# Kernel tuning notes

Hardware: AMD Instinct MI355X
Metric: run time of the kernel (lower is better)

## Reference

```python
import jax, jax.numpy as jnp
import numpy as np

N_MET = 250_000
N_RXN = 500_000
E_SUB = 2_000_000
E_ALL = 4_000_000
HIDDEN = 64
MSG_DIM = 32
DT = 0.01  # flux-limiting step size (forward called with dt > 0)


def setup_inputs() -> dict:
    key = jax.random.key(0)
    ks = jax.random.split(key, 12)
    inp = {}
    inp["x"] = jax.random.uniform(ks[0], (N_MET, 8), dtype=jnp.float32)
    inp["met_sub"] = jax.random.randint(ks[1], (E_SUB,), 0, N_MET, dtype=jnp.int32)
    inp["rxn_sub"] = jax.random.randint(ks[2], (E_SUB,), 0, N_RXN, dtype=jnp.int32)
    inp["sto_sub"] = jax.random.uniform(ks[3], (E_SUB,), dtype=jnp.float32) + 0.5  # |s_ij| > 0
    inp["met_all"] = jax.random.randint(ks[4], (E_ALL,), 0, N_MET, dtype=jnp.int32)
    inp["rxn_all"] = jax.random.randint(ks[5], (E_ALL,), 0, N_RXN, dtype=jnp.int32)
    inp["sto_all"] = jax.random.normal(ks[6], (E_ALL,), dtype=jnp.float32)
    sc = lambda fan_in: 1.0 / np.sqrt(fan_in)
    inp["W1"] = jax.random.normal(ks[7], (2, HIDDEN), dtype=jnp.float32) * sc(2)
    inp["b1"] = jnp.zeros((HIDDEN,), jnp.float32)
    inp["W2"] = jax.random.normal(ks[8], (HIDDEN, MSG_DIM), dtype=jnp.float32) * sc(HIDDEN)
    inp["b2"] = jnp.zeros((MSG_DIM,), jnp.float32)
    inp["W3"] = jax.random.normal(ks[9], (MSG_DIM, HIDDEN), dtype=jnp.float32) * sc(MSG_DIM)
    inp["b3"] = jnp.zeros((HIDDEN,), jnp.float32)
    inp["W4"] = jax.random.normal(ks[10], (HIDDEN, 1), dtype=jnp.float32) * sc(HIDDEN)
    inp["b4"] = jnp.zeros((1,), jnp.float32)
    inp["log_k"] = jax.random.uniform(ks[11], (N_RXN,), dtype=jnp.float32, minval=-3.0, maxval=-1.0)
    return inp


def reference(x, met_sub, rxn_sub, sto_sub, met_all, rxn_all, sto_all,
              W1, b1, W2, b2, W3, b3, W4, b4, log_k):
    conc = x[:, 3]                                            # [n_met]
    # per-substrate-edge message: MLP([conc_src, |s|]) -> msg_dim
    msg_in = jnp.stack([conc[met_sub], sto_sub], axis=-1)     # [E_sub, 2]
    msg = jnp.tanh(msg_in @ W1 + b1) @ W2 + b2                # [E_sub, msg_dim]
    # aggregate messages per reaction (index_add)
    h_rxn = jax.ops.segment_sum(msg, rxn_sub, num_segments=N_RXN)  # [n_rxn, msg_dim]
    # non-negative rates
    k = jnp.power(10.0, log_k)
    r = (jnp.tanh(h_rxn @ W3 + b3) @ W4 + b4)[:, 0]           # [n_rxn]
    v = k * jax.nn.softplus(r)
    # flux limiting: scale rates so no substrate is over-consumed in one dt step
    consumption = sto_sub * v[rxn_sub] * DT                   # [E_sub]
    total = jax.ops.segment_sum(consumption, met_sub, num_segments=N_MET)
    active = total > 1e-12
    met_scale = jnp.where(active,
                          jnp.minimum(conc / jnp.where(active, total, 1.0), 1.0),
                          1.0)                                # [n_met]
    edge_scale = met_scale[met_sub]
    rxn_scale = jnp.ones((N_RXN,), v.dtype).at[rxn_sub].min(edge_scale)  # amin, include_self
    v = v * rxn_scale
    # dx/dt = scatter-add of signed stoich * rate over all edges
    contrib = sto_all * v[rxn_all]                            # [E_all]
    dxdt = jax.ops.segment_sum(contrib, met_all, num_segments=N_MET)
    return dxdt[:, None]                                      # [n_met, 1]
```

## Files before the change

### kernel.cpp

```cpp
#include <hip/hip_runtime.h>

#define N_MET 250000
#define N_RXN 500000
#define N_RXN_PAD 500032
#define E_SUB 2000000
#define E_ALL 4000000
#define DT 0.01f

#define RXN_PER_BLK 256
#define THREADS 256
#define EDGE_CAP 1536

#define MV_RPB 64

#define BINSZ 1024
#define NBINS ((N_MET + BINSZ - 1) / BINSZ)
#define PART_EPB 4096
#define PTHREADS 512
#define KPB (PART_EPB / PTHREADS)
#define PART_NBLK ((E_ALL + PART_EPB - 1) / PART_EPB)
#define SPART_NBLK ((E_SUB + PART_EPB - 1) / PART_EPB)
#define RBINSZ 1024
#define RNBINS ((N_RXN + RBINSZ - 1) / RBINSZ)
#define RPART_NBLK ((E_SUB + PART_EPB - 1) / PART_EPB)
#define RBIN_CAP 6144

typedef int v4i __attribute__((ext_vector_type(4)));
typedef float v4f __attribute__((ext_vector_type(4)));
typedef short bf16x8 __attribute__((ext_vector_type(8)));
typedef float f32x4 __attribute__((ext_vector_type(4)));

#if __has_builtin(__builtin_amdgcn_exp2f)
#define EXP2F(x) __builtin_amdgcn_exp2f(x)
#else
#define EXP2F(x) exp2f(x)
#endif
#if __has_builtin(__builtin_amdgcn_rcpf)
#define RCPF(x) __builtin_amdgcn_rcpf(x)
#else
#define RCPF(x) __fdividef(1.0f, (x))
#endif

static __device__ __forceinline__ float fast_tanh(float x) {
  float e = __expf(x + x);
  return 1.0f - __fdividef(2.0f, e + 1.0f);
}

static __device__ __forceinline__ int bcast_i(int v, int lane) {
  return __builtin_amdgcn_readlane(v, lane);
}

static __device__ __forceinline__ unsigned short bf16_rn(float f) {
  unsigned u = __float_as_uint(f);
  unsigned r = u + 0x7FFFu + ((u >> 16) & 1u);
  return (unsigned short)(r >> 16);
}

__global__ __launch_bounds__(256) void k_bc3(
    const int* __restrict__ rxn_sub, const int* __restrict__ met_sub,
    const int* __restrict__ met_all,
    const float* __restrict__ x, float* __restrict__ conc,
    const float* __restrict__ W2, const float* __restrict__ W3,
    const float* __restrict__ b2,
    uint4* __restrict__ wfh, uint4* __restrict__ wfl, float* __restrict__ b2w3,
    int* __restrict__ rblk_cnt, int* __restrict__ sblk_cnt, int* __restrict__ blk_cnt) {
  __shared__ int cnt[RNBINS];
  int b = blockIdx.x, t = threadIdx.x;
  const int* keys; int nkeys, nblk, nb, bl; int* out;
  if (b < RPART_NBLK) {
    keys = rxn_sub; nkeys = E_SUB; nblk = RPART_NBLK; nb = RNBINS; out = rblk_cnt; bl = b;
    if (b < 2) {
      int tid = b * 256 + t;
      if (tid < 512) {
        int lane = tid & 63, jt = (tid >> 6) & 3, ks = tid >> 8;
        int jj = jt * 16 + (lane & 15);
        unsigned short h[8], l[8];
        #pragma unroll
        for (int q = 0; q < 8; ++q) {
          int kk = ks * 32 + (lane >> 4) * 8 + q;
          float w = 0.f;
          #pragma unroll
          for (int m = 0; m < 32; ++m) w = fmaf(W2[kk * 32 + m], W3[m * 64 + jj], w);
          h[q] = bf16_rn(w);
          float hf = __uint_as_float(((unsigned)h[q]) << 16);
          l[q] = bf16_rn(w - hf);
        }
        uint4 H, L;
        H.x = (unsigned)h[0] | ((unsigned)h[1] << 16);
        H.y = (unsigned)h[2] | ((unsigned)h[3] << 16);
        H.z = (unsigned)h[4] | ((unsigned)h[5] << 16);
        H.w = (unsigned)h[6] | ((unsigned)h[7] << 16);
        L.x = (unsigned)l[0] | ((unsigned)l[1] << 16);
        L.y = (unsigned)l[2] | ((unsigned)l[3] << 16);
        L.z = (unsigned)l[4] | ((unsigned)l[5] << 16);
        L.w = (unsigned)l[6] | ((unsigned)l[7] << 16);
        int idx = (ks * 4 + jt) * 64 + lane;
        wfh[idx] = H; wfl[idx] = L;
      }
      if (tid < 64) {
        float s = 0.f;
        #pragma unroll
        for (int m = 0; m < 32; ++m) s = fmaf(b2[m], W3[m * 64 + tid], s);
        b2w3[tid] = s;
      }
    }
  } else if (b < RPART_NBLK + SPART_NBLK) {
    keys = met_sub; nkeys = E_SUB; nblk = SPART_NBLK; nb = NBINS; out = sblk_cnt;
    bl = b - RPART_NBLK;
  } else {
    keys = met_all; nkeys = E_ALL; nblk = PART_NBLK; nb = NBINS; out = blk_cnt;
    bl = b - RPART_NBLK - SPART_NBLK;
    int m = bl * 256 + t;
    if (m < N_MET) conc[m] = __builtin_nontemporal_load(x + m * 8 + 3);
  }
  for (int i = t; i < nb; i += 256) cnt[i] = 0;
  __syncthreads();
  int base = bl * PART_EPB;
  #pragma unroll
  for (int i = 0; i < PART_EPB / 256; ++i) {
    int e = base + i * 256 + t;
    if (e < nkeys) atomicAdd(&cnt[__builtin_nontemporal_load(keys + e) >> 10], 1);
  }
  __syncthreads();
  for (int i = t; i < nb; i += 256) out[i * nblk + bl] = cnt[i];
}

static __device__ __forceinline__ void scan1_body(int* ss,
    const int* __restrict__ blk_cnt, int* __restrict__ blk_pref,
    int* __restrict__ bin_tot, int nblk, int j) {
  int t = threadIdx.x;
  int carry = 0;
  for (int c = 0; c < nblk; c += 256) {
    int idx = c + t;
    int v = (idx < nblk) ? blk_cnt[j * nblk + idx] : 0;
    ss[t] = v; __syncthreads();
    for (int d = 1; d < 256; d <<= 1) {
      int a = (t >= d) ? ss[t - d] : 0;
      __syncthreads();
      ss[t] += a;
      __syncthreads();
    }
    if (idx < nblk) blk_pref[j * nblk + idx] = carry + ss[t] - v;
    carry += ss[255];
    __syncthreads();
  }
  if (t == 0) bin_tot[j] = carry;
}

__global__ __launch_bounds__(256) void k_scan1all(
    const int* __restrict__ rblk_cnt, int* __restrict__ rblk_pref, int* __restrict__ rbin_tot,
    const int* __restrict__ sblk_cnt, int* __restrict__ sblk_pref, int* __restrict__ sbin_tot,
    const int* __restrict__ blk_cnt, int* __restrict__ blk_pref, int* __restrict__ bin_tot) {
  __shared__ int ss[256];
  int b = blockIdx.x;
  if (b < RNBINS)
    scan1_body(ss, rblk_cnt, rblk_pref, rbin_tot, RPART_NBLK, b);
  else if (b < RNBINS + NBINS)
    scan1_body(ss, sblk_cnt, sblk_pref, sbin_tot, SPART_NBLK, b - RNBINS);
  else
    scan1_body(ss, blk_cnt, blk_pref, bin_tot, PART_NBLK, b - RNBINS - NBINS);
}

__global__ __launch_bounds__(512) void k_scan2all(
    const int* __restrict__ rbin_tot, int* __restrict__ rbin_start,
    const int* __restrict__ sbin_tot, int* __restrict__ sbin_start,
    const int* __restrict__ bin_tot, int* __restrict__ bin_start) {
  __shared__ int ss[512];
  const int* tot; int* st; int n;
  if (blockIdx.x == 0)      { tot = rbin_tot; st = rbin_start; n = RNBINS; }
  else if (blockIdx.x == 1) { tot = sbin_tot; st = sbin_start; n = NBINS; }
  else                      { tot = bin_tot;  st = bin_start;  n = NBINS; }
  int t = threadIdx.x;
  int v = (t < n) ? tot[t] : 0;
  ss[t] = v; __syncthreads();
  for (int d = 1; d < 512; d <<= 1) {
    int a = (t >= d) ? ss[t - d] : 0;
    __syncthreads();
    ss[t] += a;
    __syncthreads();
  }
  if (t < n) st[t] = ss[t] - v;
}

template <int NB, bool PACK, typename MakeRec>
static __device__ __forceinline__ void part_sorted(
    const int* __restrict__ keys, int nkeys, int nblk,
    const int* __restrict__ blk_pref, const int* __restrict__ bin_start,
    int2* __restrict__ out, MakeRec make) {
  __shared__ int2 ordered[PART_EPB];
  __shared__ unsigned short binb[PACK ? 1 : PART_EPB];
  __shared__ int cnt[NB];
  __shared__ int gofs[NB];
  __shared__ int ss[PTHREADS];
  int b = blockIdx.x, t = threadIdx.x;
  for (int i = t; i < NB; i += PTHREADS) cnt[i] = 0;
  __syncthreads();
  int base = b * PART_EPB;
  int kbuf[KPB];
  #pragma unroll
  for (int i = 0; i < KPB; ++i) {
    int e = base + i * PTHREADS + t;
    kbuf[i] = (e < nkeys) ? __builtin_nontemporal_load(keys + e) : -1;
    if (kbuf[i] >= 0) atomicAdd(&cnt[kbuf[i] >> 10], 1);
  }
  __syncthreads();
  int v = (t < NB) ? cnt[t] : 0;
  ss[t] = v; __syncthreads();
  for (int d = 1; d < PTHREADS; d <<= 1) {
    int a = (t >= d) ? ss[t - d] : 0;
    __syncthreads();
    ss[t] += a;
    __syncthreads();
  }
  int nloc = ss[PTHREADS - 1];
  if (t < NB) {
    int ls = ss[t] - v;
    cnt[t] = ls;
    gofs[t] = bin_start[t] + blk_pref[t * nblk + b] - ls;
  }
  __syncthreads();
  #pragma unroll
  for (int i = 0; i < KPB; ++i) {
    int k = kbuf[i];
    if (k >= 0) {
      int e = base + i * PTHREADS + t;
      int bin = k >> 10;
      int2 rec = make(e, k);
      int pos = atomicAdd(&cnt[bin], 1);
      ordered[pos] = rec;
      if (!PACK) binb[pos] = (unsigned short)bin;
    }
  }
  __syncthreads();
  for (int i = t; i < nloc; i += PTHREADS) {
    int2 rec = ordered[i];
    int bin = PACK ? (int)(((unsigned)rec.x) >> 10) : (int)binb[i];
    out[gofs[bin] + i] = rec;
  }
}

__global__ __launch_bounds__(PTHREADS) void k_rpart(
    const int* __restrict__ rxn_sub, const int* __restrict__ met_sub,
    const float* __restrict__ sto_sub,
    const int* __restrict__ blk_pref, const int* __restrict__ bin_start,
    int2* __restrict__ bins_rxn) {
  part_sorted<RNBINS, false>(rxn_sub, E_SUB, RPART_NBLK, blk_pref, bin_start, bins_rxn,
    [=] __device__ (int e, int k) {
      int m = __builtin_nontemporal_load(met_sub + e);
      float st = __builtin_nontemporal_load(sto_sub + e);
      int2 rec; rec.x = ((k & (RBINSZ - 1)) << 18) | m; rec.y = __float_as_int(st);
      return rec;
    });
}

__global__ __launch_bounds__(PTHREADS) void k_part_sub(
    const int* __restrict__ met_sub, const int* __restrict__ rxn_sub,
    const float* __restrict__ sto_sub, const float* __restrict__ v_pre,
    const int* __restrict__ blk_pref, const int* __restrict__ bin_start,
    int2* __restrict__ bins_sub) {
  part_sorted<NBINS, true>(met_sub, E_SUB, SPART_NBLK, blk_pref, bin_start, bins_sub,
    [=] __device__ (int e, int k) {
      int r = __builtin_nontemporal_load(rxn_sub + e);
      float st = __builtin_nontemporal_load(sto_sub + e);
      float val = st * v_pre[r] * DT;
      int2 rec; rec.x = k; rec.y = __float_as_int(val);
      return rec;
    });
}

__global__ __launch_bounds__(PTHREADS) void k_part(
    const int* __restrict__ met_all, const int* __restrict__ rxn_all,
    const float* __restrict__ sto_all, const float* __restrict__ vfin,
    const int* __restrict__ blk_pref, const int* __restrict__ bin_start,
    int2* __restrict__ bins) {
  part_sorted<NBINS, true>(met_all, E_ALL, PART_NBLK, blk_pref, bin_start, bins,
    [=] __device__ (int e, int k) {
      int r = __builtin_nontemporal_load(rxn_all + e);
      float st = __builtin_nontemporal_load(sto_all + e);
      float val = st * vfin[r];
      int2 rec; rec.x = k; rec.y = __float_as_int(val);
      return rec;
    });
}

__global__ __launch_bounds__(256) void k_rbin(
    const int2* __restrict__ bins_rxn, const int* __restrict__ rbin_start,
    const int* __restrict__ rbin_tot, int2* __restrict__ edges8, int* __restrict__ off) {
  __shared__ int2 stage[RBIN_CAP];
  __shared__ int lcnt[RBINSZ];
  __shared__ int lcur[RBINSZ];
  __shared__ int ss[256];
  int j = blockIdx.x, t = threadIdx.x;
  int base = rbin_start[j], n = rbin_tot[j];
  for (int i = t; i < RBINSZ; i += 256) lcnt[i] = 0;
  __syncthreads();
  bool fits = (n <= RBIN_CAP);
  if (fits) {
    for (int i = t; i < n; i += 256) {
      int2 rec = bins_rxn[base + i];
      stage[i] = rec;
      atomicAdd(&lcnt[((unsigned)rec.x) >> 18], 1);
    }
  } else {
    for (int i = t; i < n; i += 256) {
      int2 rec = bins_rxn[base + i];
      atomicAdd(&lcnt[((unsigned)rec.x) >> 18], 1);
    }
  }
  __syncthreads();
  int s0 = lcnt[4 * t], s1 = lcnt[4 * t + 1], s2 = lcnt[4 * t + 2], s3 = lcnt[4 * t + 3];
  int tsum = s0 + s1 + s2 + s3;
  ss[t] = tsum; __syncthreads();
  for (int d = 1; d < 256; d <<= 1) {
    int a = (t >= d) ? ss[t - d] : 0;
    __syncthreads();
    ss[t] += a;
    __syncthreads();
  }
  int run = ss[t] - tsum;
  lcur[4 * t] = run;
  lcur[4 * t + 1] = run + s0;
  lcur[4 * t + 2] = run + s0 + s1;
  lcur[4 * t + 3] = run + s0 + s1 + s2;
  __syncthreads();
  int R0 = j * RBINSZ;
  for (int rl = t; rl < RBINSZ; rl += 256) {
    int r = R0 + rl;
    if (r < N_RXN) off[r] = base + lcur[rl];
  }
  if (j == 0 && t == 0) off[N_RXN] = E_SUB;
  __syncthreads();
  if (fits) {
    for (int i = t; i < n; i += 256) {
      int2 rec = stage[i];
      int pos = atomicAdd(&lcur[((unsigned)rec.x) >> 18], 1);
      int2 out; out.x = rec.x & 0x3FFFF; out.y = rec.y;
      edges8[base + pos] = out;
    }
  } else {
    for (int i = t; i < n; i += 256) {
      int2 rec = bins_rxn[base + i];
      int pos = atomicAdd(&lcur[((unsigned)rec.x) >> 18], 1);
      int2 out; out.x = rec.x & 0x3FFFF; out.y = rec.y;
      edges8[base + pos] = out;
    }
  }
}

static __device__ __forceinline__ float edge_rsum_lds(int o0, int o1, int estart,
                                                      const float2* ep,
                                                      float w1x, float w1y, float b1j) {
  float S0 = 0.f, S1 = 0.f;
  int c = o0;
  for (; c + 1 < o1; c += 2) {
    float2 e0 = ep[c - estart];
    float2 e1 = ep[c + 1 - estart];
    float t0 = fmaf(e0.x, w1x, fmaf(e0.y, w1y, b1j));
    float t1 = fmaf(e1.x, w1x, fmaf(e1.y, w1y, b1j));
    S0 += RCPF(EXP2F(t0) + 1.0f);
    S1 += RCPF(EXP2F(t1) + 1.0f);
  }
  if (c < o1) {
    float2 e0 = ep[c - estart];
    float t0 = fmaf(e0.x, w1x, fmaf(e0.y, w1y, b1j));
    S0 += RCPF(EXP2F(t0) + 1.0f);
  }
  return S0 + S1;
}

static __device__ __forceinline__ float edge_rsum_glob(int o0, int o1,
                                                       const int2* edges8,
                                                       const float* conc,
                                                       float w1x, float w1y, float b1j) {
  float S = 0.f;
  for (int c = o0; c < o1; ++c) {
    int2 rec = edges8[c];
    float cc = conc[rec.x];
    float t0 = fmaf(cc, w1x, fmaf(__int_as_float(rec.y), w1y, b1j));
    S += RCPF(EXP2F(t0) + 1.0f);
  }
  return S;
}

__global__ __launch_bounds__(THREADS) void k_edge(
    const int* __restrict__ off, const int2* __restrict__ edges8,
    const float* __restrict__ conc,
    const float* __restrict__ W1, const float* __restrict__ b1,
    unsigned short* __restrict__ Thi, unsigned short* __restrict__ Tlo, int use_lo) {
  __shared__ int off_s[RXN_PER_BLK + 1];
  __shared__ float2 se[EDGE_CAP];

  int tid = threadIdx.x;
  int lane = tid & 63;
  int wv = tid >> 6;
  int R0 = blockIdx.x * RXN_PER_BLK;

  for (int i = tid; i <= RXN_PER_BLK; i += THREADS) {
    int r = R0 + i;
    off_s[i] = off[r > N_RXN ? N_RXN : r];
  }
  __syncthreads();
  int estart = off_s[0];
  int nE = off_s[RXN_PER_BLK] - estart;
  bool fits = (nE <= EDGE_CAP);
  if (fits) {
    for (int i = tid; i < nE; i += THREADS) {
      int2 rec = edges8[estart + i];
      se[i] = make_float2(conc[rec.x], __int_as_float(rec.y));
    }
  }

  const float C2 = 2.8853900817779268f;
  float w1x = W1[lane] * C2, w1y = W1[64 + lane] * C2, b1j = b1[lane] * C2;

  int rbase = R0 + wv * 64;
  int o0l = off_s[wv * 64 + lane];
  int o1l = off_s[wv * 64 + lane + 1];

  __syncthreads();

  int o0 = bcast_i(o0l, 0);
  #pragma clang loop unroll(disable)
  for (int i = 0; i < 64; ++i) {
    int r = rbase + i;
    if (r >= N_RXN) break;
    int o1 = bcast_i(o1l, i);
    float S = fits ? edge_rsum_lds(o0, o1, estart, se, w1x, w1y, b1j)
                   : edge_rsum_glob(o0, o1, edges8, conc, w1x, w1y, b1j);
    float T = (float)(o1 - o0) - 2.0f * S;
    unsigned short hi = bf16_rn(T);
    Thi[r * 64 + lane] = hi;
    if (use_lo) {
      float hf = __uint_as_float(((unsigned)hi) << 16);
      Tlo[r * 64 + lane] = bf16_rn(T - hf);
    }
    o0 = o1;
  }
}

__global__ __launch_bounds__(256) void k_mv(
    const int* __restrict__ off,
    const unsigned short* __restrict__ Thi, const unsigned short* __restrict__ Tlo,
    const uint4* __restrict__ wfh, const uint4* __restrict__ wfl,
    const float* __restrict__ b2w3, const float* __restrict__ b3,
    const float* __restrict__ W4, const float* __restrict__ b4,
    const float* __restrict__ log_k, int use_lo, float* __restrict__ v_pre) {
  __shared__ int soff[MV_RPB + 1];
  int tid = threadIdx.x, lane = tid & 63, w = tid >> 6;
  int B0 = blockIdx.x * MV_RPB;
  for (int i = tid; i <= MV_RPB; i += 256) {
    int r = B0 + i;
    soff[i] = off[r > N_RXN ? N_RXN : r];
  }
  __syncthreads();

  int R0 = B0 + w * 16;
  int col = lane & 15, rowg = lane >> 4;

  bf16x8 ah[2], al[2];
  {
    int rowelem = (R0 + col) * 64 + rowg * 8;
    const uint4* ph = (const uint4*)Thi;
    ah[0] = __builtin_bit_cast(bf16x8, ph[rowelem >> 3]);
    ah[1] = __builtin_bit_cast(bf16x8, ph[(rowelem + 32) >> 3]);
    if (use_lo) {
      const uint4* pl = (const uint4*)Tlo;
      al[0] = __builtin_bit_cast(bf16x8, pl[rowelem >> 3]);
      al[1] = __builtin_bit_cast(bf16x8, pl[(rowelem + 32) >> 3]);
    }
  }

  f32x4 acc[4];
  #pragma unroll
  for (int jt = 0; jt < 4; ++jt) acc[jt] = (f32x4){0.f, 0.f, 0.f, 0.f};

  #pragma unroll
  for (int jt = 0; jt < 4; ++jt) {
    #pragma unroll
    for (int ks = 0; ks < 2; ++ks) {
      int bidx = (ks * 4 + jt) * 64 + lane;
      bf16x8 bh = __builtin_bit_cast(bf16x8, wfh[bidx]);
      acc[jt] = __builtin_amdgcn_mfma_f32_16x16x32_bf16(ah[ks], bh, acc[jt], 0, 0, 0);
      if (use_lo) {
        bf16x8 bl = __builtin_bit_cast(bf16x8, wfl[bidx]);
        acc[jt] = __builtin_amdgcn_mfma_f32_16x16x32_bf16(ah[ks], bl, acc[jt], 0, 0, 0);
        acc[jt] = __builtin_amdgcn_mfma_f32_16x16x32_bf16(al[ks], bh, acc[jt], 0, 0, 0);
      }
    }
  }

  float w4c[4], bwc[4], b3c[4];
  #pragma unroll
  for (int jt = 0; jt < 4; ++jt) {
    int jj = jt * 16 + col;
    w4c[jt] = W4[jj]; bwc[jt] = b2w3[jj]; b3c[jt] = b3[jj];
  }
  float b40 = b4[0];

  float nq[4];
  #pragma unroll
  for (int q = 0; q < 4; ++q) {
    int idx = w * 16 + rowg * 4 + q;
    nq[q] = (float)(soff[idx + 1] - soff[idx]);
  }

  #pragma unroll
  for (int q = 0; q < 4; ++q) {
    float s = 0.f;
    #pragma unroll
    for (int jt = 0; jt < 4; ++jt) {
      float u = acc[jt][q] + nq[q] * bwc[jt] + b3c[jt];
      s += fast_tanh(u) * w4c[jt];
    }
    s += __shfl_xor(s, 1, 64);
    s += __shfl_xor(s, 2, 64);
    s += __shfl_xor(s, 4, 64);
    s += __shfl_xor(s, 8, 64);
    if (col == 0) {
      int r = R0 + rowg * 4 + q;
      float lk = (r < N_RXN) ? log_k[r] : 0.f;
      float racc = s + b40;
      float k10 = __expf(lk * 2.3025850929940457f);
      float sp = (racc > 15.f) ? racc : __logf(1.f + __expf(racc));
      if (r < N_RXN) v_pre[r] = k10 * sp;
    }
  }
}

__global__ __launch_bounds__(512) void k_bins_sub(
    const int2* __restrict__ bins_sub, const int* __restrict__ bin_start,
    const int* __restrict__ bin_tot, const float* __restrict__ conc,
    float* __restrict__ met_scale) {
  __shared__ float acc[BINSZ];
  int j = blockIdx.x, t = threadIdx.x;
  for (int i = t; i < BINSZ; i += 512) acc[i] = 0.f;
  __syncthreads();
  int s0 = bin_start[j], n = bin_tot[j];
  for (int i = t; i < n; i += 512) {
    int2 rec = bins_sub[s0 + i];
    atomicAdd(&acc[rec.x & (BINSZ - 1)], __int_as_float(rec.y));
  }
  __syncthreads();
  int m0 = j * BINSZ;
  for (int i = t; i < BINSZ; i += 512) {
    int m = m0 + i;
    if (m < N_MET) {
      float tot = acc[i];
      met_scale[m] = (tot > 1e-12f) ? fminf(conc[m] / tot, 1.0f) : 1.0f;
    }
  }
}

__global__ __launch_bounds__(256) void k_rscale(
    const int* __restrict__ off, const int2* __restrict__ edges8,
    const float* __restrict__ met_scale, const float* __restrict__ v_pre,
    float* __restrict__ vfin) {
  __shared__ int soff[MV_RPB + 1];
  int tid = threadIdx.x, lane = tid & 63, w = tid >> 6;
  int B0 = blockIdx.x * MV_RPB;
  for (int i = tid; i <= MV_RPB; i += 256) {
    int r = B0 + i;
    soff[i] = off[r > N_RXN ? N_RXN : r];
  }
  __syncthreads();

  int rloc = w * 16 + (lane >> 2);
  int o0 = soff[rloc], o1 = soff[rloc + 1];
  float sc = 1.0f;
  for (int c = o0 + (lane & 3); c < o1; c += 4) {
    sc = fminf(sc, met_scale[edges8[c].x]);
  }
  sc = fminf(sc, __shfl_xor(sc, 1, 64));
  sc = fminf(sc, __shfl_xor(sc, 2, 64));
  if ((lane & 3) == 0) {
    int r = B0 + rloc;
    if (r < N_RXN) vfin[r] = v_pre[r] * sc;
  }
}

__global__ __launch_bounds__(512) void k_bins(const int2* __restrict__ bins,
                                              const int* __restrict__ bin_start,
                                              const int* __restrict__ bin_tot,
                                              float* __restrict__ dxdt) {
  __shared__ float acc[BINSZ];
  int j = blockIdx.x, t = threadIdx.x;
  for (int i = t; i < BINSZ; i += 512) acc[i] = 0.f;
  __syncthreads();
  int s0 = bin_start[j], n = bin_tot[j];
  for (int i = t; i < n; i += 512) {
    int2 rec = bins[s0 + i];
    atomicAdd(&acc[rec.x & (BINSZ - 1)], __int_as_float(rec.y));
  }
  __syncthreads();
  int m0 = j * BINSZ;
  for (int i = t; i < BINSZ; i += 512) {
    int m = m0 + i;
    if (m < N_MET) dxdt[m] = acc[i];
  }
}

extern "C" void kernel_launch(void* const* d_in, const int* in_sizes, int n_in,
                              void* d_out, int out_size, void* d_ws, size_t ws_size,
                              hipStream_t stream) {
  const float* x       = (const float*)d_in[0];
  const int*   met_sub = (const int*)d_in[1];
  const int*   rxn_sub = (const int*)d_in[2];
  const float* sto_sub = (const float*)d_in[3];
  const int*   met_all = (const int*)d_in[4];
  const int*   rxn_all = (const int*)d_in[5];
  const float* sto_all = (const float*)d_in[6];
  const float* W1    = (const float*)d_in[7];
  const float* b1    = (const float*)d_in[8];
  const float* W2    = (const float*)d_in[9];
  const float* b2    = (const float*)d_in[10];
  const float* W3    = (const float*)d_in[11];
  const float* b3    = (const float*)d_in[12];
  const float* W4    = (const float*)d_in[13];
  const float* b4    = (const float*)d_in[14];
  const float* log_k = (const float*)d_in[15];
  float* dxdt = (float*)d_out;

  char* ws = (char*)d_ws;
  size_t p = 0;
  auto alloc = [&](size_t bytes) -> void* {
    void* r = (void*)(ws + p);
    p += (bytes + 255) & ~(size_t)255;
    return r;
  };
  int*    off        = (int*)alloc(sizeof(int) * (N_RXN + 1));
  uint4*  wfh        = (uint4*)alloc(sizeof(uint4) * 512);
  uint4*  wfl        = (uint4*)alloc(sizeof(uint4) * 512);
  float*  b2w3       = (float*)alloc(sizeof(float) * 64);
  float*  v_pre      = (float*)alloc(sizeof(float) * N_RXN);
  float*  vfin       = (float*)alloc(sizeof(float) * N_RXN);
  float*  conc       = (float*)alloc(sizeof(float) * N_MET);
  float*  met_scale  = (float*)alloc(sizeof(float) * N_MET);
  int2*   edges8     = (int2*)alloc(sizeof(int2) * E_SUB);
  int2*   bins_rxn   = (int2*)alloc(sizeof(int2) * E_SUB);
  int2*   bins_sub   = (int2*)alloc(sizeof(int2) * E_SUB);
  int2*   bins       = (int2*)alloc(sizeof(int2) * E_ALL);
  int*    rblk_cnt   = (int*)alloc(sizeof(int) * RNBINS * RPART_NBLK);
  int*    rblk_pref  = (int*)alloc(sizeof(int) * RNBINS * RPART_NBLK);
  int*    sblk_cnt   = (int*)alloc(sizeof(int) * NBINS * SPART_NBLK);
  int*    sblk_pref  = (int*)alloc(sizeof(int) * NBINS * SPART_NBLK);
  int*    blk_cnt    = (int*)alloc(sizeof(int) * NBINS * PART_NBLK);
  int*    blk_pref   = (int*)alloc(sizeof(int) * NBINS * PART_NBLK);
  int*    rbin_tot   = (int*)alloc(sizeof(int) * 512);
  int*    rbin_start = (int*)alloc(sizeof(int) * 512);
  int*    sbin_tot   = (int*)alloc(sizeof(int) * 512);
  int*    sbin_start = (int*)alloc(sizeof(int) * 512);
  int*    bin_tot    = (int*)alloc(sizeof(int) * 512);
  int*    bin_start  = (int*)alloc(sizeof(int) * 512);
  unsigned short* Thi = (unsigned short*)alloc(sizeof(unsigned short) * (size_t)N_RXN_PAD * 64);
  size_t tlo_bytes = sizeof(unsigned short) * (size_t)N_RXN_PAD * 64;
  int use_lo = (p + tlo_bytes <= ws_size) ? 1 : 0;
  unsigned short* Tlo = use_lo ? (unsigned short*)alloc(tlo_bytes) : Thi;
  (void)in_sizes; (void)n_in; (void)out_size;


  k_bc3<<<RPART_NBLK + SPART_NBLK + PART_NBLK, 256, 0, stream>>>(
      rxn_sub, met_sub, met_all, x, conc, W2, W3, b2, wfh, wfl, b2w3,
      rblk_cnt, sblk_cnt, blk_cnt);
  k_scan1all<<<RNBINS + NBINS + NBINS, 256, 0, stream>>>(
      rblk_cnt, rblk_pref, rbin_tot, sblk_cnt, sblk_pref, sbin_tot,
      blk_cnt, blk_pref, bin_tot);
  k_scan2all<<<3, 512, 0, stream>>>(rbin_tot, rbin_start, sbin_tot, sbin_start,
                                    bin_tot, bin_start);

  k_rpart<<<RPART_NBLK, PTHREADS, 0, stream>>>(rxn_sub, met_sub, sto_sub,
                                               rblk_pref, rbin_start, bins_rxn);
  k_rbin<<<RNBINS, 256, 0, stream>>>(bins_rxn, rbin_start, rbin_tot, edges8, off);

  k_edge<<<(N_RXN + RXN_PER_BLK - 1) / RXN_PER_BLK, THREADS, 0, stream>>>(
      off, edges8, conc, W1, b1, Thi, Tlo, use_lo);
  k_mv<<<(N_RXN + MV_RPB - 1) / MV_RPB, 256, 0, stream>>>(
      off, Thi, Tlo, wfh, wfl, b2w3, b3, W4, b4, log_k, use_lo, v_pre);

  k_part_sub<<<SPART_NBLK, PTHREADS, 0, stream>>>(met_sub, rxn_sub, sto_sub, v_pre,
                                                  sblk_pref, sbin_start, bins_sub);
  k_bins_sub<<<NBINS, 512, 0, stream>>>(bins_sub, sbin_start, sbin_tot, conc, met_scale);

  k_rscale<<<(N_RXN + MV_RPB - 1) / MV_RPB, 256, 0, stream>>>(
      off, edges8, met_scale, v_pre, vfin);

  k_part<<<PART_NBLK, PTHREADS, 0, stream>>>(met_all, rxn_all, sto_all, vfin,
                                             blk_pref, bin_start, bins);
  k_bins<<<NBINS, 512, 0, stream>>>(bins, bin_start, bin_tot, dxdt);
}
```

Before: 430.3 us.

## Fuse edge-sum and MFMA rate kernels through per-wave LDS tiles

Merges the per-reaction edge tanh-sum kernel with the MFMA matrix-vector rate kernel. Each wave now writes its 16-reaction T tile (hi and lo bf16 parts) into padded shared memory and runs the MFMAs immediately, so the 500k x 64 bf16 intermediates never go to global memory. This removes a kernel launch and two large global round trips. In exchange the fused kernel uses more LDS and registers, which may lower occupancy, and the lo correction is now always computed.

After: 418.9 us. 1.03x faster.

```diff
diff --git a/kernel.cpp b/kernel.cpp
--- a/kernel.cpp
+++ b/kernel.cpp
@@ -2,7 +2,6 @@
 
 #define N_MET 250000
 #define N_RXN 500000
-#define N_RXN_PAD 500032
 #define E_SUB 2000000
 #define E_ALL 4000000
 #define DT 0.01f
@@ -10,6 +9,7 @@
 #define RXN_PER_BLK 256
 #define THREADS 256
 #define EDGE_CAP 1536
+#define TPAD 72
 
 #define MV_RPB 64
 
@@ -382,13 +382,18 @@
   return S;
 }
 
-__global__ __launch_bounds__(THREADS) void k_edge(
+__global__ __launch_bounds__(THREADS) void k_edge_mv(
     const int* __restrict__ off, const int2* __restrict__ edges8,
     const float* __restrict__ conc,
     const float* __restrict__ W1, const float* __restrict__ b1,
-    unsigned short* __restrict__ Thi, unsigned short* __restrict__ Tlo, int use_lo) {
+    const uint4* __restrict__ wfh, const uint4* __restrict__ wfl,
+    const float* __restrict__ b2w3, const float* __restrict__ b3,
+    const float* __restrict__ W4, const float* __restrict__ b4,
+    const float* __restrict__ log_k, float* __restrict__ v_pre) {
   __shared__ int off_s[RXN_PER_BLK + 1];
   __shared__ float2 se[EDGE_CAP];
+  __shared__ __align__(16) unsigned short thi[4][16][TPAD];
+  __shared__ __align__(16) unsigned short tlo[4][16][TPAD];
 
   int tid = threadIdx.x;
   int lane = tid & 63;
@@ -417,77 +422,7 @@
   int o0l = off_s[wv * 64 + lane];
   int o1l = off_s[wv * 64 + lane + 1];
 
-  __syncthreads();
-
-  int o0 = bcast_i(o0l, 0);
-  #pragma clang loop unroll(disable)
-  for (int i = 0; i < 64; ++i) {
-    int r = rbase + i;
-    if (r >= N_RXN) break;
-    int o1 = bcast_i(o1l, i);
-    float S = fits ? edge_rsum_lds(o0, o1, estart, se, w1x, w1y, b1j)
-                   : edge_rsum_glob(o0, o1, edges8, conc, w1x, w1y, b1j);
-    float T = (float)(o1 - o0) - 2.0f * S;
-    unsigned short hi = bf16_rn(T);
-    Thi[r * 64 + lane] = hi;
-    if (use_lo) {
-      float hf = __uint_as_float(((unsigned)hi) << 16);
-      Tlo[r * 64 + lane] = bf16_rn(T - hf);
-    }
-    o0 = o1;
-  }
-}
-
-__global__ __launch_bounds__(256) void k_mv(
-    const int* __restrict__ off,
-    const unsigned short* __restrict__ Thi, const unsigned short* __restrict__ Tlo,
-    const uint4* __restrict__ wfh, const uint4* __restrict__ wfl,
-    const float* __restrict__ b2w3, const float* __restrict__ b3,
-    const float* __restrict__ W4, const float* __restrict__ b4,
-    const float* __restrict__ log_k, int use_lo, float* __restrict__ v_pre) {
-  __shared__ int soff[MV_RPB + 1];
-  int tid = threadIdx.x, lane = tid & 63, w = tid >> 6;
-  int B0 = blockIdx.x * MV_RPB;
-  for (int i = tid; i <= MV_RPB; i += 256) {
-    int r = B0 + i;
-    soff[i] = off[r > N_RXN ? N_RXN : r];
-  }
-  __syncthreads();
-
-  int R0 = B0 + w * 16;
   int col = lane & 15, rowg = lane >> 4;
-
-  bf16x8 ah[2], al[2];
-  {
-    int rowelem = (R0 + col) * 64 + rowg * 8;
-    const uint4* ph = (const uint4*)Thi;
-    ah[0] = __builtin_bit_cast(bf16x8, ph[rowelem >> 3]);
-    ah[1] = __builtin_bit_cast(bf16x8, ph[(rowelem + 32) >> 3]);
-    if (use_lo) {
-      const uint4* pl = (const uint4*)Tlo;
-      al[0] = __builtin_bit_cast(bf16x8, pl[rowelem >> 3]);
-      al[1] = __builtin_bit_cast(bf16x8, pl[(rowelem + 32) >> 3]);
-    }
-  }
-
-  f32x4 acc[4];
-  #pragma unroll
-  for (int jt = 0; jt < 4; ++jt) acc[jt] = (f32x4){0.f, 0.f, 0.f, 0.f};
-
-  #pragma unroll
-  for (int jt = 0; jt < 4; ++jt) {
-    #pragma unroll
-    for (int ks = 0; ks < 2; ++ks) {
-      int bidx = (ks * 4 + jt) * 64 + lane;
-      bf16x8 bh = __builtin_bit_cast(bf16x8, wfh[bidx]);
-      acc[jt] = __builtin_amdgcn_mfma_f32_16x16x32_bf16(ah[ks], bh, acc[jt], 0, 0, 0);
-      if (use_lo) {
-        bf16x8 bl = __builtin_bit_cast(bf16x8, wfl[bidx]);
-        acc[jt] = __builtin_amdgcn_mfma_f32_16x16x32_bf16(ah[ks], bl, acc[jt], 0, 0, 0);
-        acc[jt] = __builtin_amdgcn_mfma_f32_16x16x32_bf16(al[ks], bh, acc[jt], 0, 0, 0);
-      }
-    }
-  }
 
   float w4c[4], bwc[4], b3c[4];
   #pragma unroll
@@ -497,32 +432,83 @@
   }
   float b40 = b4[0];
 
-  float nq[4];
-  #pragma unroll
-  for (int q = 0; q < 4; ++q) {
-    int idx = w * 16 + rowg * 4 + q;
-    nq[q] = (float)(soff[idx + 1] - soff[idx]);
-  }
-
-  #pragma unroll
-  for (int q = 0; q < 4; ++q) {
-    float s = 0.f;
+  __syncthreads();
+
+  const uint4* wfh_v = wfh;
+  const uint4* wfl_v = wfl;
+
+  unsigned short* thw = &thi[wv][0][0];
+  unsigned short* tlw = &tlo[wv][0][0];
+
+  int o0 = bcast_i(o0l, 0);
+  #pragma clang loop unroll(disable)
+  for (int tt = 0; tt < 4; ++tt) {
+    asm volatile("" : "+v"(wfh_v), "+v"(wfl_v));
+    int rt = rbase + tt * 16;
+    #pragma clang loop unroll(disable)
+    for (int i = 0; i < 16; ++i) {
+      int li = tt * 16 + i;
+      int o1 = bcast_i(o1l, li);
+      float S = fits ? edge_rsum_lds(o0, o1, estart, se, w1x, w1y, b1j)
+                     : edge_rsum_glob(o0, o1, edges8, conc, w1x, w1y, b1j);
+      float T = (float)(o1 - o0) - 2.0f * S;
+      unsigned short hi = bf16_rn(T);
+      float hf = __uint_as_float(((unsigned)hi) << 16);
+      thw[i * TPAD + lane] = hi;
+      tlw[i * TPAD + lane] = bf16_rn(T - hf);
+      o0 = o1;
+    }
+    bf16x8 ah[2], al[2];
+    {
+      int fo = col * TPAD + rowg * 8;
+      const uint4* ph = (const uint4*)thw;
+      const uint4* pl = (const uint4*)tlw;
+      ah[0] = __builtin_bit_cast(bf16x8, ph[fo >> 3]);
+      ah[1] = __builtin_bit_cast(bf16x8, ph[(fo + 32) >> 3]);
+      al[0] = __builtin_bit_cast(bf16x8, pl[fo >> 3]);
+      al[1] = __builtin_bit_cast(bf16x8, pl[(fo + 32) >> 3]);
+    }
+    f32x4 acc[4];
+    #pragma unroll
+    for (int jt = 0; jt < 4; ++jt) acc[jt] = (f32x4){0.f, 0.f, 0.f, 0.f};
     #pragma unroll
     for (int jt = 0; jt < 4; ++jt) {
-      float u = acc[jt][q] + nq[q] * bwc[jt] + b3c[jt];
-      s += fast_tanh(u) * w4c[jt];
-    }
-    s += __shfl_xor(s, 1, 64);
-    s += __shfl_xor(s, 2, 64);
-    s += __shfl_xor(s, 4, 64);
-    s += __shfl_xor(s, 8, 64);
-    if (col == 0) {
-      int r = R0 + rowg * 4 + q;
-      float lk = (r < N_RXN) ? log_k[r] : 0.f;
-      float racc = s + b40;
-      float k10 = __expf(lk * 2.3025850929940457f);
-      float sp = (racc > 15.f) ? racc : __logf(1.f + __expf(racc));
-      if (r < N_RXN) v_pre[r] = k10 * sp;
+      #pragma unroll
+      for (int ks = 0; ks < 2; ++ks) {
+        int bidx = (ks * 4 + jt) * 64 + lane;
+        bf16x8 bh = __builtin_bit_cast(bf16x8, wfh_v[bidx]);
+        bf16x8 bl = __builtin_bit_cast(bf16x8, wfl_v[bidx]);
+        acc[jt] = __builtin_amdgcn_mfma_f32_16x16x32_bf16(ah[ks], bh, acc[jt], 0, 0, 0);
+        acc[jt] = __builtin_amdgcn_mfma_f32_16x16x32_bf16(ah[ks], bl, acc[jt], 0, 0, 0);
+        acc[jt] = __builtin_amdgcn_mfma_f32_16x16x32_bf16(al[ks], bh, acc[jt], 0, 0, 0);
+      }
+    }
+    float nq[4];
+    #pragma unroll
+    for (int q = 0; q < 4; ++q) {
+      int idx = tt * 16 + rowg * 4 + q + wv * 64;
+      nq[q] = (float)(off_s[idx + 1] - off_s[idx]);
+    }
+    #pragma unroll
+    for (int q = 0; q < 4; ++q) {
+      float s = 0.f;
+      #pragma unroll
+      for (int jt = 0; jt < 4; ++jt) {
+        float u = acc[jt][q] + nq[q] * bwc[jt] + b3c[jt];
+        s += fast_tanh(u) * w4c[jt];
+      }
+      s += __shfl_xor(s, 1, 64);
+      s += __shfl_xor(s, 2, 64);
+      s += __shfl_xor(s, 4, 64);
+      s += __shfl_xor(s, 8, 64);
+      if (col == 0) {
+        int r = rt + rowg * 4 + q;
+        float lk = (r < N_RXN) ? log_k[r] : 0.f;
+        float racc = s + b40;
+        float k10 = __expf(lk * 2.3025850929940457f);
+        float sp = (racc > 15.f) ? racc : __logf(1.f + __expf(racc));
+        if (r < N_RXN) v_pre[r] = k10 * sp;
+      }
     }
   }
 }
@@ -651,11 +637,7 @@
   int*    sbin_start = (int*)alloc(sizeof(int) * 512);
   int*    bin_tot    = (int*)alloc(sizeof(int) * 512);
   int*    bin_start  = (int*)alloc(sizeof(int) * 512);
-  unsigned short* Thi = (unsigned short*)alloc(sizeof(unsigned short) * (size_t)N_RXN_PAD * 64);
-  size_t tlo_bytes = sizeof(unsigned short) * (size_t)N_RXN_PAD * 64;
-  int use_lo = (p + tlo_bytes <= ws_size) ? 1 : 0;
-  unsigned short* Tlo = use_lo ? (unsigned short*)alloc(tlo_bytes) : Thi;
-  (void)in_sizes; (void)n_in; (void)out_size;
+  (void)in_sizes; (void)n_in; (void)out_size; (void)ws_size;
 
 
   k_bc3<<<RPART_NBLK + SPART_NBLK + PART_NBLK, 256, 0, stream>>>(
@@ -671,10 +653,8 @@
                                                rblk_pref, rbin_start, bins_rxn);
   k_rbin<<<RNBINS, 256, 0, stream>>>(bins_rxn, rbin_start, rbin_tot, edges8, off);
 
-  k_edge<<<(N_RXN + RXN_PER_BLK - 1) / RXN_PER_BLK, THREADS, 0, stream>>>(
-      off, edges8, conc, W1, b1, Thi, Tlo, use_lo);
-  k_mv<<<(N_RXN + MV_RPB - 1) / MV_RPB, 256, 0, stream>>>(
-      off, Thi, Tlo, wfh, wfl, b2w3, b3, W4, b4, log_k, use_lo, v_pre);
+  k_edge_mv<<<(N_RXN + RXN_PER_BLK - 1) / RXN_PER_BLK, THREADS, 0, stream>>>(
+      off, edges8, conc, W1, b1, wfh, wfl, b2w3, b3, W4, b4, log_k, v_pre);
 
   k_part_sub<<<SPART_NBLK, PTHREADS, 0, stream>>>(met_sub, rxn_sub, sto_sub, v_pre,
                                                   sblk_pref, sbin_start, bins_sub);
```
